# Kernel optimization log

Hardware: AMD Instinct MI355X
Metric: run time of the kernel (lower is better)

Reference implementation:

```python
import jax, jax.numpy as jnp
import numpy as np

N, E, F, H = 20000, 320000, 128, 256   # nodes, edges, in-features, hidden
M, NQ = 4096, 2048                      # lsq rows, QP variables
LAMB_MAX = 2.0


def setup_inputs() -> dict:
    key = jax.random.key(0)
    ks = jax.random.split(key, 12)
    x = jax.random.normal(ks[0], (N, F), jnp.float32)
    edge_index = jax.random.randint(ks[1], (2, E), 0, N)
    A = jax.random.normal(ks[2], (M, NQ), jnp.float32) * 0.05
    b = jax.random.normal(ks[3], (M, 1), jnp.float32)
    feat_ids = jax.random.randint(ks[4], (NQ,), 0, N)
    x_prior = jax.random.uniform(ks[5], (NQ, 1), jnp.float32)
    lamb = jnp.ones((1,), jnp.float32)
    # ChebConv K=2 weights: one linear per Chebyshev order, plus bias
    W10 = jax.random.normal(ks[6], (F, H), jnp.float32) / np.sqrt(F)
    W11 = jax.random.normal(ks[7], (F, H), jnp.float32) / np.sqrt(F)
    b1 = jnp.zeros((H,), jnp.float32)
    W20 = jax.random.normal(ks[8], (H, 1), jnp.float32) / np.sqrt(H)
    W21 = jax.random.normal(ks[9], (H, 1), jnp.float32) / np.sqrt(H)
    b2 = jnp.zeros((1,), jnp.float32)
    return {"x": x, "edge_index": edge_index, "A": A, "b": b,
            "feat_ids": feat_ids, "x_prior": x_prior, "lamb": lamb,
            "W10": W10, "W11": W11, "b1": b1,
            "W20": W20, "W21": W21, "b2": b2}


def _cheb_conv(x, edge_index, W0, W1, bias, lam_max):
    """PyG ChebConv with K=2: out = x @ W0 + (2L/lam_max - I) x @ W1 + bias,
    L = I - D^{-1/2} A D^{-1/2}, via edge gather/scatter (no dense NxN)."""
    row, col = edge_index[0], edge_index[1]
    n = x.shape[0]
    deg = jax.ops.segment_sum(jnp.ones_like(row, dtype=x.dtype), row, num_segments=n)
    dinv = jnp.where(deg > 0, deg ** -0.5, 0.0)
    # normalized edge weight scaled by 2/lam_max, negated (off-diag of L_hat)
    w = -(2.0 / lam_max) * dinv[row] * dinv[col]              # [E]
    msg = jax.ops.segment_sum(w[:, None] * x[col], row, num_segments=n)
    Tx1 = msg + (2.0 / lam_max - 1.0) * x                      # diagonal of L_hat
    return x @ W0 + Tx1 @ W1 + bias


def reference(x, edge_index, A, b, feat_ids, x_prior, lamb,
              W10, W11, b1, W20, W21, b2):
    h = jax.nn.relu(_cheb_conv(x, edge_index, W10, W11, b1, LAMB_MAX))
    h = lamb[0] * jax.nn.relu(_cheb_conv(h, edge_index, W20, W21, b2, LAMB_MAX))
    hfold = h[feat_ids] + 1e-5                                 # [NQ, 1]
    q = hfold[:, 0]
    # QP: min 1/2 z^T Q z + p^T z with vacuous inequality (0*z <= 0.1) and no
    # equality constraints -> interior-point converges to unconstrained min.
    Q = A.T @ A + jnp.diag(q)                                  # [NQ, NQ]
    p = -(x_prior * hfold)[:, 0] - (b.T @ A)[0]                # [NQ]
    z = jnp.linalg.solve(Q, -p)                                # [NQ]
    return z[:, None]                                          # f.T -> [NQ, 1]
```

## Files before the change

kernel.cpp:

```cpp
#include <hip/hip_runtime.h>

#define N_NODES 20000
#define N_EDGES 320000
#define F_DIM   128
#define H_DIM   256
#define M_ROWS  4096
#define NQ      2048
#define NIT     18
#define MM_ROWS 20032

typedef __attribute__((ext_vector_type(8))) short short8;
typedef __attribute__((ext_vector_type(4))) float f32x4;


__device__ __forceinline__ float wred(float v) {
#pragma unroll
  for (int m = 32; m > 0; m >>= 1) v += __shfl_xor(v, m, 64);
  return v;
}

__device__ __forceinline__ float bred256(float v, float* lds) {
  v = wred(v);
  int w = threadIdx.x >> 6;
  if ((threadIdx.x & 63) == 0) lds[w] = v;
  __syncthreads();
  float tot = lds[0] + lds[1] + lds[2] + lds[3];
  __syncthreads();
  return tot;
}

__device__ __forceinline__ unsigned f2bf(float f) {
  unsigned u = __float_as_uint(f);
  unsigned r = u + 0x7fffu + ((u >> 16) & 1u);
  return r >> 16;
}
__device__ __forceinline__ float bflo(unsigned u) { return __uint_as_float(u << 16); }
__device__ __forceinline__ float bfhi(unsigned u) { return __uint_as_float(u & 0xffff0000u); }


__global__ __launch_bounds__(1024) void k_scan(const int* __restrict__ deg,
    int* __restrict__ rowstart, float* __restrict__ dinv) {
  __shared__ int part[1024];
  int t = threadIdx.x;
  const int chunk = (N_NODES + 1023) / 1024;
  int lo = t * chunk;
  int hi = lo + chunk; if (hi > N_NODES) hi = N_NODES;
  int s = 0;
  for (int i = lo; i < hi; ++i) {
    int d = deg[i];
    dinv[i] = d > 0 ? rsqrtf((float)d) : 0.f;
    s += d;
  }
  part[t] = s;
  __syncthreads();
  for (int off = 1; off < 1024; off <<= 1) {
    int v = part[t];
    int add = (t >= off) ? part[t - off] : 0;
    __syncthreads();
    part[t] = v + add;
    __syncthreads();
  }
  int base = (t > 0) ? part[t - 1] : 0;
  for (int i = lo; i < hi; ++i) { rowstart[i] = base; base += deg[i]; }
  if (t == 0) rowstart[N_NODES] = part[1023];
}

__global__ __launch_bounds__(256) void k_scatter(const int* __restrict__ ei,
    const int* __restrict__ rowstart, int* __restrict__ cursor,
    const float* __restrict__ dinv, int* __restrict__ cols, float* __restrict__ wvals) {
  int e = blockIdx.x * 256 + threadIdx.x;
  if (e >= N_EDGES) return;
  int r = ei[e];
  int c = ei[N_EDGES + e];
  int pos = rowstart[r] + atomicAdd(&cursor[r], 1);
  cols[pos] = c;
  wvals[pos] = -dinv[r] * dinv[c];
}

#define CONVX_BLKS (MM_ROWS * 16 / 256)
#define DEG_BLKS   ((N_EDGES + 255) / 256)
#define PREP_BASE  (CONVX_BLKS + 128 + DEG_BLKS)

__global__ __launch_bounds__(256) void k_pack(const float* __restrict__ x,
    const float* __restrict__ W10, const float* __restrict__ W11,
    unsigned* __restrict__ xu, unsigned* __restrict__ Wtb,
    const int* __restrict__ ei, int* __restrict__ deg,
    const float* __restrict__ A, const float* __restrict__ b,
    unsigned* __restrict__ Atu, float* __restrict__ btA_parts) {
  int bx = blockIdx.x;
  if (bx < CONVX_BLKS) {
    int gid = bx * 256 + threadIdx.x;
    int row = gid >> 4;
    int q8 = gid & 15;
    uint4* xu4 = (uint4*)xu;
    if (row < N_NODES) {
      const float4* x4 = (const float4*)x;
      float4 a = x4[(size_t)row * 32 + q8 * 2];
      float4 b2 = x4[(size_t)row * 32 + q8 * 2 + 1];
      uint4 u;
      u.x = f2bf(a.x) | (f2bf(a.y) << 16);
      u.y = f2bf(a.z) | (f2bf(a.w) << 16);
      u.z = f2bf(b2.x) | (f2bf(b2.y) << 16);
      u.w = f2bf(b2.z) | (f2bf(b2.w) << 16);
      xu4[(size_t)row * 32 + q8] = u;
    } else {
      uint4 z = make_uint4(0, 0, 0, 0);
      xu4[(size_t)row * 32 + q8] = z;
      xu4[(size_t)row * 32 + 16 + q8] = z;
    }
  } else if (bx < CONVX_BLKS + 128) {
    int gid = (bx - CONVX_BLKS) * 256 + threadIdx.x;
    int n = gid >> 7;
    int u = gid & 127;
    int k0 = u * 2;
    float v0 = (k0 < 128) ? W10[(size_t)k0 * H_DIM + n]
                          : W11[(size_t)(k0 - 128) * H_DIM + n];
    float v1 = (k0 + 1 < 128) ? W10[(size_t)(k0 + 1) * H_DIM + n]
                              : W11[(size_t)(k0 - 127) * H_DIM + n];
    Wtb[(size_t)n * 128 + u] = f2bf(v0) | (f2bf(v1) << 16);
  } else if (bx < PREP_BASE) {
    int e = (bx - CONVX_BLKS - 128) * 256 + threadIdx.x;
    if (e < N_EDGES) atomicAdd(&deg[ei[e]], 1);
  } else {
    const int pb = bx - PREP_BASE;
    int jp = (pb & 3) * 256 + threadIdx.x;
    int k0 = (pb >> 2) * 128;
    const float2* A2 = (const float2*)A;
    float acc0 = 0.f, acc1 = 0.f;
    for (int kk = 0; kk < 128; kk += 8) {
      float ax[8], ay[8];
#pragma unroll
      for (int i = 0; i < 8; ++i) {
        int k = k0 + kk + i;
        float2 a = A2[(size_t)k * 1024 + jp];
        float bk = b[k];
        acc0 += a.x * bk;
        acc1 += a.y * bk;
        ax[i] = a.x; ay[i] = a.y;
      }
      uint4 t0, t1;
      t0.x = f2bf(ax[0]) | (f2bf(ax[1]) << 16);
      t0.y = f2bf(ax[2]) | (f2bf(ax[3]) << 16);
      t0.z = f2bf(ax[4]) | (f2bf(ax[5]) << 16);
      t0.w = f2bf(ax[6]) | (f2bf(ax[7]) << 16);
      t1.x = f2bf(ay[0]) | (f2bf(ay[1]) << 16);
      t1.y = f2bf(ay[2]) | (f2bf(ay[3]) << 16);
      t1.z = f2bf(ay[4]) | (f2bf(ay[5]) << 16);
      t1.w = f2bf(ay[6]) | (f2bf(ay[7]) << 16);
      int uoff = (k0 + kk) >> 1;
      *(uint4*)(Atu + (size_t)(2 * jp) * 2048 + uoff) = t0;
      *(uint4*)(Atu + (size_t)(2 * jp + 1) * 2048 + uoff) = t1;
    }
    ((float2*)(btA_parts + (size_t)(pb >> 2) * NQ))[jp] = make_float2(acc0, acc1);
  }
}

__global__ __launch_bounds__(256) void k_msg1(const int* __restrict__ rowstart,
    const int* __restrict__ cols, const float* __restrict__ wvals,
    unsigned* __restrict__ xu) {
  int wid = (blockIdx.x * 256 + threadIdx.x) >> 6;
  int lane = threadIdx.x & 63;
  if (wid >= N_NODES) return;
  int s0 = rowstart[wid], s1 = rowstart[wid + 1];
  float2 a0 = make_float2(0.f, 0.f), a1 = make_float2(0.f, 0.f);
  float2 a2 = make_float2(0.f, 0.f), a3 = make_float2(0.f, 0.f);
  int e = s0;
  for (; e + 4 <= s1; e += 4) {
    int c0 = cols[e], c1 = cols[e + 1], c2 = cols[e + 2], c3 = cols[e + 3];
    float w0 = wvals[e], w1 = wvals[e + 1], w2 = wvals[e + 2], w3 = wvals[e + 3];
    unsigned u0 = xu[(size_t)c0 * 128 + lane];
    unsigned u1 = xu[(size_t)c1 * 128 + lane];
    unsigned u2 = xu[(size_t)c2 * 128 + lane];
    unsigned u3 = xu[(size_t)c3 * 128 + lane];
    a0.x += w0 * bflo(u0); a0.y += w0 * bfhi(u0);
    a1.x += w1 * bflo(u1); a1.y += w1 * bfhi(u1);
    a2.x += w2 * bflo(u2); a2.y += w2 * bfhi(u2);
    a3.x += w3 * bflo(u3); a3.y += w3 * bfhi(u3);
  }
  for (; e < s1; ++e) {
    int c = cols[e];
    float w = wvals[e];
    unsigned u = xu[(size_t)c * 128 + lane];
    a0.x += w * bflo(u); a0.y += w * bfhi(u);
  }
  float ax = (a0.x + a1.x) + (a2.x + a3.x);
  float ay = (a0.y + a1.y) + (a2.y + a3.y);
  xu[(size_t)wid * 128 + 64 + lane] = f2bf(ax) | (f2bf(ay) << 16);
}


__device__ __forceinline__ void mm_ldfrag(short8* Af, short8* Bf,
    const unsigned* __restrict__ xurow, const unsigned* __restrict__ wrow, int kc) {
#pragma unroll
  for (int a = 0; a < 4; ++a)
    Af[a] = *(const short8*)(xurow + (size_t)a * 16 * 128 + kc * 16);
#pragma unroll
  for (int n = 0; n < 4; ++n)
    Bf[n] = *(const short8*)(wrow + (size_t)n * 16 * 128 + kc * 16);
}

__global__ __launch_bounds__(256) void k_mm(const unsigned* __restrict__ xu,
    const unsigned* __restrict__ Wtb, const float* __restrict__ b1,
    const float* __restrict__ W20, const float* __restrict__ W21,
    float* __restrict__ t, float* __restrict__ s) {
  const int row0 = blockIdx.x * 64;
  const int tid = threadIdx.x;
  const int w = tid >> 6, lane = tid & 63;
  const int colb = w * 64;
  const int frow = lane & 15, fqo = (lane >> 4) * 4;
  const int c16 = lane & 15, q4 = lane >> 4;

  f32x4 acc[4][4];
#pragma unroll
  for (int a = 0; a < 4; ++a)
#pragma unroll
    for (int b = 0; b < 4; ++b) {
      acc[a][b][0] = 0.f; acc[a][b][1] = 0.f;
      acc[a][b][2] = 0.f; acc[a][b][3] = 0.f;
    }

  const unsigned* xurow = xu + (size_t)(row0 + frow) * 128 + fqo;
  const unsigned* wrow  = Wtb + (size_t)(colb + frow) * 128 + fqo;

  short8 A0[4], B0[4], A1[4], B1[4];
  mm_ldfrag(A0, B0, xurow, wrow, 0);
#pragma unroll
  for (int kp = 0; kp < 4; ++kp) {
    const int kc = kp * 2;
    mm_ldfrag(A1, B1, xurow, wrow, kc + 1);
#pragma unroll
    for (int a = 0; a < 4; ++a)
#pragma unroll
      for (int n = 0; n < 4; ++n)
        acc[a][n] = __builtin_amdgcn_mfma_f32_16x16x32_bf16(A0[a], B0[n], acc[a][n], 0, 0, 0);
    if (kc + 2 < 8) mm_ldfrag(A0, B0, xurow, wrow, kc + 2);
#pragma unroll
    for (int a = 0; a < 4; ++a)
#pragma unroll
      for (int n = 0; n < 4; ++n)
        acc[a][n] = __builtin_amdgcn_mfma_f32_16x16x32_bf16(A1[a], B1[n], acc[a][n], 0, 0, 0);
  }

  float tp[4][4] = {}, sp[4][4] = {};
#pragma unroll
  for (int b2 = 0; b2 < 4; ++b2) {
    int gc = colb + b2 * 16 + c16;
    float w20 = W20[gc], w21 = W21[gc], bb = b1[gc];
#pragma unroll
    for (int a = 0; a < 4; ++a)
#pragma unroll
      for (int r = 0; r < 4; ++r) {
        float val = acc[a][b2][r] + bb;
        val = val > 0.f ? val : 0.f;
        tp[a][r] += val * w20;
        sp[a][r] += val * w21;
      }
  }
#pragma unroll
  for (int a = 0; a < 4; ++a)
#pragma unroll
    for (int r = 0; r < 4; ++r) {
#pragma unroll
      for (int m = 1; m < 16; m <<= 1) {
        tp[a][r] += __shfl_xor(tp[a][r], m, 64);
        sp[a][r] += __shfl_xor(sp[a][r], m, 64);
      }
    }
  if (c16 == 0) {
#pragma unroll
    for (int a = 0; a < 4; ++a)
#pragma unroll
      for (int r = 0; r < 4; ++r) {
        int gr = row0 + a * 16 + q4 * 4 + r;
        if (gr < N_NODES) {
          atomicAdd(&t[gr], tp[a][r]);
          atomicAdd(&s[gr], sp[a][r]);
        }
      }
  }
}


__global__ __launch_bounds__(256) void k_h2(const float* __restrict__ t,
    const float* __restrict__ s, const int* __restrict__ rowstart,
    const int* __restrict__ cols, const float* __restrict__ wvals,
    const float* __restrict__ lamb, const float* __restrict__ b2, float* __restrict__ h2) {
  int i = blockIdx.x * 256 + threadIdx.x;
  if (i >= N_NODES) return;
  int s0 = rowstart[i], s1 = rowstart[i + 1];
  float m0 = 0.f, m1 = 0.f, m2 = 0.f, m3 = 0.f;
  int e = s0;
  for (; e + 4 <= s1; e += 4) {
    int c0 = cols[e], c1 = cols[e + 1], c2 = cols[e + 2], c3 = cols[e + 3];
    float w0 = wvals[e], w1 = wvals[e + 1], w2 = wvals[e + 2], w3 = wvals[e + 3];
    m0 += w0 * s[c0];
    m1 += w1 * s[c1];
    m2 += w2 * s[c2];
    m3 += w3 * s[c3];
  }
  for (; e < s1; ++e) m0 += wvals[e] * s[cols[e]];
  float m = (m0 + m1) + (m2 + m3);
  float val = t[i] + m + b2[0];
  val = val > 0.f ? val : 0.f;
  h2[i] = lamb[0] * val;
}

#define GR_ST2 36
#define NTILE 136

__global__ __launch_bounds__(512) void k_gram(const unsigned* __restrict__ Atu,
    float* __restrict__ Gp,
    const float* __restrict__ h2, const int* __restrict__ feat_ids,
    const float* __restrict__ x_prior, const float* __restrict__ btA_parts,
    float* __restrict__ q, float* __restrict__ r0) {
  if (blockIdx.x >= 544) {
    if (threadIdx.x < 256) {
      int j = (blockIdx.x - 544) * 256 + threadIdx.x;
      int f = feat_ids[j];
      float hf = h2[f] + 1e-5f;
      q[j] = hf;
      float bta = 0.f;
#pragma unroll
      for (int c = 0; c < 32; ++c) bta += btA_parts[(size_t)c * NQ + j];
      r0[j] = x_prior[j] * hf + bta;
    }
    return;
  }
  __shared__ unsigned shA[128 * GR_ST2];
  __shared__ unsigned shB[128 * GR_ST2];
  const int bid = blockIdx.x;
  const int wid = (bid & 7) * 68 + (bid >> 3);
  const int tile = wid >> 2;
  const int kq = wid & 3;
  int uu = tile, bi = 0;
  while (uu >= 16 - bi) { uu -= 16 - bi; ++bi; }
  const int bj = bi + uu;
  const int i0 = bi * 128, j0 = bj * 128;
  const int tid = threadIdx.x;
  const int w = tid >> 6, lane = tid & 63;
  const int wr = (w >> 2) * 64, wc = (w & 3) * 32;
  const int srow = tid >> 2, sua = (tid & 3) * 8;
  const int frow = lane & 15, fqo = (lane >> 4) * 4;

  f32x4 acc[4][2];
#pragma unroll
  for (int a = 0; a < 4; ++a)
#pragma unroll
    for (int b = 0; b < 2; ++b) {
      acc[a][b][0] = 0.f; acc[a][b][1] = 0.f;
      acc[a][b][2] = 0.f; acc[a][b][3] = 0.f;
    }

  const unsigned* pa = Atu + (size_t)(i0 + srow) * 2048 + kq * 512 + sua;
  const unsigned* pb = Atu + (size_t)(j0 + srow) * 2048 + kq * 512 + sua;

  uint4 pra0 = *(const uint4*)(pa);
  uint4 pra1 = *(const uint4*)(pa + 4);
  uint4 prb0 = *(const uint4*)(pb);
  uint4 prb1 = *(const uint4*)(pb + 4);

  unsigned* as = shA + srow * GR_ST2 + sua;
  unsigned* bs = shB + srow * GR_ST2 + sua;

  for (int sp = 0; sp < 16; ++sp) {
    *(uint4*)as = pra0; *(uint4*)(as + 4) = pra1;
    *(uint4*)bs = prb0; *(uint4*)(bs + 4) = prb1;
    if (sp + 1 < 16) {
      const int ku = (sp + 1) * 32;
      pra0 = *(const uint4*)(pa + ku);
      pra1 = *(const uint4*)(pa + ku + 4);
      prb0 = *(const uint4*)(pb + ku);
      prb1 = *(const uint4*)(pb + ku + 4);
    }
    __syncthreads();
#pragma unroll
    for (int kk = 0; kk < 2; ++kk) {
      short8 af[4], bf[2];
#pragma unroll
      for (int a = 0; a < 4; ++a)
        af[a] = *(const short8*)(shA + (wr + a * 16 + frow) * GR_ST2 + kk * 16 + fqo);
#pragma unroll
      for (int b2 = 0; b2 < 2; ++b2)
        bf[b2] = *(const short8*)(shB + (wc + b2 * 16 + frow) * GR_ST2 + kk * 16 + fqo);
#pragma unroll
      for (int a = 0; a < 4; ++a)
#pragma unroll
        for (int b2 = 0; b2 < 2; ++b2)
          acc[a][b2] = __builtin_amdgcn_mfma_f32_16x16x32_bf16(af[a], bf[b2], acc[a][b2], 0, 0, 0);
    }
    __syncthreads();
  }

  const int q4 = lane >> 4, c16 = lane & 15;
  float* Gz = Gp + ((size_t)kq * NTILE + tile) * 16384;
#pragma unroll
  for (int a = 0; a < 4; ++a)
#pragma unroll
    for (int b2 = 0; b2 < 2; ++b2)
#pragma unroll
      for (int r = 0; r < 4; ++r) {
        int lr = wr + a * 16 + q4 * 4 + r;
        int lc = wc + b2 * 16 + c16;
        Gz[lr * 128 + lc] = acc[a][b2][r];
      }
}

#define GT_ST 131

__global__ __launch_bounds__(256) void k_gconv(const float* __restrict__ Gp,
    const float* __restrict__ q, unsigned* __restrict__ Gb, float* __restrict__ qcorr) {
  __shared__ unsigned short T[128 * GT_ST];
  int uu = blockIdx.x, bi = 0;
  while (uu >= 16 - bi) { uu -= 16 - bi; ++bi; }
  const int bj = bi + uu;
  const int tid = threadIdx.x;
  const int r = tid >> 1, ch = (tid & 1) * 64;
  const size_t tile = (size_t)blockIdx.x * 16384;
  const float4* P0 = (const float4*)(Gp + tile + r * 128 + ch);
  const float4* P1 = (const float4*)(Gp + (size_t)1 * NTILE * 16384 + tile + r * 128 + ch);
  const float4* P2 = (const float4*)(Gp + (size_t)2 * NTILE * 16384 + tile + r * 128 + ch);
  const float4* P3 = (const float4*)(Gp + (size_t)3 * NTILE * 16384 + tile + r * 128 + ch);
  const int gr = bi * 128 + r;
  const bool hasdiag = (bi == bj) && (r >= ch) && (r < ch + 64);
  unsigned uo[32];
#pragma unroll
  for (int j = 0; j < 16; ++j) {
    float4 a = P0[j], b = P1[j], c = P2[j], d = P3[j];
    float v0 = a.x + b.x + c.x + d.x;
    float v1 = a.y + b.y + c.y + d.y;
    float v2 = a.z + b.z + c.z + d.z;
    float v3 = a.w + b.w + c.w + d.w;
    const int c0 = ch + j * 4;
    if (hasdiag && (r - c0 >= 0) && (r - c0 < 4)) {
      float qv = q[gr];
      int dsel = r - c0;
      if (dsel == 0) v0 += qv;
      else if (dsel == 1) v1 += qv;
      else if (dsel == 2) v2 += qv;
      else v3 += qv;
      float vd = (dsel == 0) ? v0 : (dsel == 1) ? v1 : (dsel == 2) ? v2 : v3;
      qcorr[gr] = vd - bflo(f2bf(vd));
    }
    unsigned u0 = f2bf(v0) | (f2bf(v1) << 16);
    unsigned u1 = f2bf(v2) | (f2bf(v3) << 16);
    uo[2 * j] = u0;
    uo[2 * j + 1] = u1;
    T[r * GT_ST + c0]     = (unsigned short)(u0 & 0xffffu);
    T[r * GT_ST + c0 + 1] = (unsigned short)(u0 >> 16);
    T[r * GT_ST + c0 + 2] = (unsigned short)(u1 & 0xffffu);
    T[r * GT_ST + c0 + 3] = (unsigned short)(u1 >> 16);
  }
  uint4* dst = (uint4*)(Gb + (size_t)gr * 1024 + bj * 64 + (ch >> 1));
#pragma unroll
  for (int j = 0; j < 8; ++j) dst[j] = ((const uint4*)uo)[j];
  __syncthreads();
  if (bi != bj) {
    const int wv = tid >> 6, lane = tid & 63;
    for (int kk = 0; kk < 32; ++kk) {
      int rr = kk * 4 + wv;
      unsigned lo = T[(2 * lane) * GT_ST + rr];
      unsigned hi = T[(2 * lane + 1) * GT_ST + rr];
      Gb[(size_t)(bj * 128 + rr) * 1024 + bi * 64 + lane] = lo | (hi << 16);
    }
  }
}

__global__ __launch_bounds__(256) void k_cgG(int k, const unsigned* __restrict__ Gb,
    const float* __restrict__ qcorr,
    const float* __restrict__ r_old, float* __restrict__ r_new,
    const float* __restrict__ p_old, float* __restrict__ p_new,
    const float* __restrict__ Qp_in, float* __restrict__ Qp_out,
    float* __restrict__ xcg) {
  __shared__ float pshare[NQ];
  __shared__ float lds[4];
  const int tid = threadIdx.x, bid = blockIdx.x;
  const float4* r4 = (const float4*)r_old;
  float4 ra = r4[tid * 2], rb2 = r4[tid * 2 + 1];
  float pv[8];
  if (k == 0) {
    pv[0] = ra.x; pv[1] = ra.y; pv[2] = ra.z; pv[3] = ra.w;
    pv[4] = rb2.x; pv[5] = rb2.y; pv[6] = rb2.z; pv[7] = rb2.w;
    if (bid == 0) {
      ((float4*)p_new)[tid * 2] = ra;
      ((float4*)p_new)[tid * 2 + 1] = rb2;
    }
  } else {
    const float4* p4 = (const float4*)p_old;
    const float4* qp4 = (const float4*)Qp_in;
    float4 pa = p4[tid * 2], pb = p4[tid * 2 + 1];
    float4 qa = qp4[tid * 2], qb = qp4[tid * 2 + 1];
    float rr = ra.x * ra.x + ra.y * ra.y + ra.z * ra.z + ra.w * ra.w +
               rb2.x * rb2.x + rb2.y * rb2.y + rb2.z * rb2.z + rb2.w * rb2.w;
    float pap = pa.x * qa.x + pa.y * qa.y + pa.z * qa.z + pa.w * qa.w +
                pb.x * qb.x + pb.y * qb.y + pb.z * qb.z + pb.w * qb.w;
    rr = bred256(rr, lds);
    pap = bred256(pap, lds);
    float alpha = rr / pap;
    if (bid == 0) {
      float4* x4 = (float4*)xcg;
      float4 xa = x4[tid * 2], xb = x4[tid * 2 + 1];
      xa.x += alpha * pa.x; xa.y += alpha * pa.y;
      xa.z += alpha * pa.z; xa.w += alpha * pa.w;
      xb.x += alpha * pb.x; xb.y += alpha * pb.y;
      xb.z += alpha * pb.z; xb.w += alpha * pb.w;
      x4[tid * 2] = xa; x4[tid * 2 + 1] = xb;
    }
    ra.x -= alpha * qa.x; ra.y -= alpha * qa.y;
    ra.z -= alpha * qa.z; ra.w -= alpha * qa.w;
    rb2.x -= alpha * qb.x; rb2.y -= alpha * qb.y;
    rb2.z -= alpha * qb.z; rb2.w -= alpha * qb.w;
    float rrn = ra.x * ra.x + ra.y * ra.y + ra.z * ra.z + ra.w * ra.w +
                rb2.x * rb2.x + rb2.y * rb2.y + rb2.z * rb2.z + rb2.w * rb2.w;
    rrn = bred256(rrn, lds);
    float beta = rrn / rr;
    pv[0] = ra.x + beta * pa.x; pv[1] = ra.y + beta * pa.y;
    pv[2] = ra.z + beta * pa.z; pv[3] = ra.w + beta * pa.w;
    pv[4] = rb2.x + beta * pb.x; pv[5] = rb2.y + beta * pb.y;
    pv[6] = rb2.z + beta * pb.z; pv[7] = rb2.w + beta * pb.w;
    if (bid == 0) {
      ((float4*)r_new)[tid * 2] = ra;
      ((float4*)r_new)[tid * 2 + 1] = rb2;
      ((float4*)p_new)[tid * 2] = make_float4(pv[0], pv[1], pv[2], pv[3]);
      ((float4*)p_new)[tid * 2 + 1] = make_float4(pv[4], pv[5], pv[6], pv[7]);
    }
  }
  ((float4*)pshare)[tid * 2] = make_float4(pv[0], pv[1], pv[2], pv[3]);
  ((float4*)pshare)[tid * 2 + 1] = make_float4(pv[4], pv[5], pv[6], pv[7]);
  __syncthreads();
  const int w = tid >> 6, lane = tid & 63;
  const int row0 = bid * 8 + w * 2;
  const uint4* Gr0 = (const uint4*)(Gb + (size_t)row0 * 1024);
  const uint4* Gr1 = (const uint4*)(Gb + (size_t)(row0 + 1) * 1024);
  const float4* ps4 = (const float4*)pshare;
  float acc0 = 0.f, acc1 = 0.f;
#pragma unroll
  for (int c = 0; c < 4; ++c) {
    uint4 g0 = Gr0[c * 64 + lane];
    uint4 g1 = Gr1[c * 64 + lane];
    float4 pa = ps4[c * 128 + lane * 2];
    float4 pb = ps4[c * 128 + lane * 2 + 1];
    acc0 += bflo(g0.x) * pa.x + bfhi(g0.x) * pa.y;
    acc0 += bflo(g0.y) * pa.z + bfhi(g0.y) * pa.w;
    acc0 += bflo(g0.z) * pb.x + bfhi(g0.z) * pb.y;
    acc0 += bflo(g0.w) * pb.z + bfhi(g0.w) * pb.w;
    acc1 += bflo(g1.x) * pa.x + bfhi(g1.x) * pa.y;
    acc1 += bflo(g1.y) * pa.z + bfhi(g1.y) * pa.w;
    acc1 += bflo(g1.z) * pb.x + bfhi(g1.z) * pb.y;
    acc1 += bflo(g1.w) * pb.z + bfhi(g1.w) * pb.w;
  }
  acc0 = wred(acc0);
  acc1 = wred(acc1);
  if (lane == 0) {
    Qp_out[row0] = acc0 + qcorr[row0] * pshare[row0];
    Qp_out[row0 + 1] = acc1 + qcorr[row0 + 1] * pshare[row0 + 1];
  }
}

__global__ __launch_bounds__(256) void k_cgfin(const float* __restrict__ r_last,
    const float* __restrict__ p_last, const float* __restrict__ Qp,
    const float* __restrict__ xcg, float* __restrict__ out) {
  const int tid = threadIdx.x;
  const int lane = tid & 63;
  const float4* r4 = (const float4*)r_last;
  const float4* p4 = (const float4*)p_last;
  const float4* q4 = (const float4*)Qp;
  float rr = 0.f, pap = 0.f;
#pragma unroll
  for (int c = 0; c < 4; ++c) {
#pragma unroll
    for (int hh = 0; hh < 2; ++hh) {
      float4 rv = r4[c * 128 + lane * 2 + hh];
      float4 pv = p4[c * 128 + lane * 2 + hh];
      float4 qv = q4[c * 128 + lane * 2 + hh];
      rr += rv.x * rv.x + rv.y * rv.y + rv.z * rv.z + rv.w * rv.w;
      pap += pv.x * qv.x + pv.y * qv.y + pv.z * qv.z + pv.w * qv.w;
    }
  }
  rr = wred(rr);
  pap = wred(pap);
  float alpha = rr / pap;
  const float4* x4 = (const float4*)xcg;
  float4* o4 = (float4*)out;
#pragma unroll
  for (int hh = 0; hh < 2; ++hh) {
    int i4 = tid * 2 + hh;
    float4 xv = x4[i4];
    float4 pv = p4[i4];
    xv.x += alpha * pv.x; xv.y += alpha * pv.y;
    xv.z += alpha * pv.z; xv.w += alpha * pv.w;
    o4[i4] = xv;
  }
}


extern "C" void kernel_launch(void* const* d_in, const int* in_sizes, int n_in,
                              void* d_out, int out_size, void* d_ws, size_t ws_size,
                              hipStream_t stream) {
  const float* x      = (const float*)d_in[0];
  const int*   ei     = (const int*)d_in[1];
  const float* A      = (const float*)d_in[2];
  const float* b      = (const float*)d_in[3];
  const int*   fids   = (const int*)d_in[4];
  const float* xprior = (const float*)d_in[5];
  const float* lamb   = (const float*)d_in[6];
  const float* W10    = (const float*)d_in[7];
  const float* W11    = (const float*)d_in[8];
  const float* b1     = (const float*)d_in[9];
  const float* W20    = (const float*)d_in[10];
  const float* W21    = (const float*)d_in[11];
  const float* b2     = (const float*)d_in[12];
  float* out = (float*)d_out;

  char* base = (char*)d_ws;
  size_t o = 0;
  auto alloc = [&](size_t bytes) { size_t r = o; o = (o + bytes + 255) & ~size_t(255); return r; };

  size_t off_deg    = alloc(N_NODES * 4);
  size_t off_cursor = alloc(N_NODES * 4);
  size_t off_xcg    = alloc(NQ * 4);
  size_t off_t      = alloc(N_NODES * 4);
  size_t off_s      = alloc(N_NODES * 4);
  size_t zero_end   = o;
  size_t off_rowst  = alloc((N_NODES + 1) * 4);
  size_t off_dinv   = alloc(N_NODES * 4);
  size_t off_h2     = alloc(N_NODES * 4);
  size_t off_q      = alloc(NQ * 4);
  size_t off_r0     = alloc(NQ * 4);
  size_t off_r1     = alloc(NQ * 4);
  size_t off_p0     = alloc(NQ * 4);
  size_t off_p1     = alloc(NQ * 4);
  size_t off_Qp0    = alloc(NQ * 4);
  size_t off_Qp1    = alloc(NQ * 4);
  size_t off_qcorr  = alloc(NQ * 4);
  size_t off_btAp   = alloc(32 * NQ * 4);
  size_t off_Wtb    = alloc(256 * 128 * 4);
  size_t sz_cols  = (size_t)N_EDGES * 4 + 256;
  size_t sz_wvals = (size_t)N_EDGES * 4 + 256;
  size_t sz_xmsg  = (size_t)MM_ROWS * 256 * 2;
  size_t union_gnn = sz_cols + sz_wvals + sz_xmsg;
  size_t sz_gb     = (size_t)NQ * NQ * 2;
  size_t off_union = alloc(union_gnn > sz_gb ? union_gnn : sz_gb);
  size_t off_atu   = alloc((size_t)M_ROWS * NQ * 2);
  size_t off_Gp    = alloc((size_t)4 * NTILE * 16384 * 4);
  if (o > ws_size) return;

  int*   deg      = (int*)(base + off_deg);
  int*   cursor   = (int*)(base + off_cursor);
  float* xcg      = (float*)(base + off_xcg);
  float* t        = (float*)(base + off_t);
  float* s        = (float*)(base + off_s);
  int*   rowstart = (int*)(base + off_rowst);
  float* dinv     = (float*)(base + off_dinv);
  float* h2       = (float*)(base + off_h2);
  float* q        = (float*)(base + off_q);
  float* rb[2]    = {(float*)(base + off_r0), (float*)(base + off_r1)};
  float* pg[2]    = {(float*)(base + off_p0), (float*)(base + off_p1)};
  float* Qpb[2]   = {(float*)(base + off_Qp0), (float*)(base + off_Qp1)};
  float* qcorr    = (float*)(base + off_qcorr);
  float* btA_parts = (float*)(base + off_btAp);
  unsigned* Wtb   = (unsigned*)(base + off_Wtb);
  int*   cols     = (int*)(base + off_union);
  float* wvals    = (float*)(base + off_union + sz_cols);
  unsigned* xmsgb = (unsigned*)(base + off_union + sz_cols + sz_wvals);
  unsigned* Gb    = (unsigned*)(base + off_union);
  unsigned* Atu   = (unsigned*)(base + off_atu);
  float* Gp       = (float*)(base + off_Gp);

  hipMemsetAsync(d_ws, 0, zero_end, stream);

  k_pack<<<PREP_BASE + 128, 256, 0, stream>>>(x, W10, W11, xmsgb, Wtb, ei, deg,
                                              A, b, Atu, btA_parts);
  k_scan<<<1, 1024, 0, stream>>>(deg, rowstart, dinv);
  k_scatter<<<DEG_BLKS, 256, 0, stream>>>(ei, rowstart, cursor, dinv, cols, wvals);

  k_msg1<<<N_NODES / 4, 256, 0, stream>>>(rowstart, cols, wvals, xmsgb);
  k_mm<<<MM_ROWS / 64, 256, 0, stream>>>(xmsgb, Wtb, b1, W20, W21, t, s);
  k_h2<<<(N_NODES + 255) / 256, 256, 0, stream>>>(t, s, rowstart, cols, wvals, lamb, b2, h2);

  k_gram<<<552, 512, 0, stream>>>(Atu, Gp, h2, fids, xprior, btA_parts, q, rb[0]);
  k_gconv<<<NTILE, 256, 0, stream>>>(Gp, q, Gb, qcorr);

  k_cgG<<<256, 256, 0, stream>>>(0, Gb, qcorr, rb[0], rb[0], pg[0], pg[0],
                                 Qpb[1], Qpb[0], xcg);
  for (int k = 1; k < NIT; ++k) {
    k_cgG<<<256, 256, 0, stream>>>(k, Gb, qcorr, rb[(k - 1) & 1], rb[k & 1],
                                   pg[(k - 1) & 1], pg[k & 1],
                                   Qpb[(k - 1) & 1], Qpb[k & 1], xcg);
  }
  k_cgfin<<<1, 256, 0, stream>>>(rb[(NIT - 1) & 1], pg[(NIT - 1) & 1],
                                 Qpb[(NIT - 1) & 1], xcg, out);
}
```

Before: 397.4 us.

## Move A transpose/pack into separate LDS-tiled kernel after conv matmul

Moves the A-transpose-to-bf16 and b^T A partial computation out of the fused k_pack kernel into a new k_prep2 kernel. The new kernel stages a 128x64 tile in shared memory so both the global reads of A and the packed writes of Atu are coalesced, where the old per-thread loop issued strided 16-byte stores. It is launched after k_mm, taking A's packing off the critical path of the graph preprocessing. The cost is one extra kernel launch and a separate pass that no longer overlaps with the edge-degree work.

```diff
diff --git a/kernel.cpp b/kernel.cpp
--- a/kernel.cpp
+++ b/kernel.cpp
@@ -79,14 +79,11 @@
 
 #define CONVX_BLKS (MM_ROWS * 16 / 256)
 #define DEG_BLKS   ((N_EDGES + 255) / 256)
-#define PREP_BASE  (CONVX_BLKS + 128 + DEG_BLKS)
 
 __global__ __launch_bounds__(256) void k_pack(const float* __restrict__ x,
     const float* __restrict__ W10, const float* __restrict__ W11,
     unsigned* __restrict__ xu, unsigned* __restrict__ Wtb,
-    const int* __restrict__ ei, int* __restrict__ deg,
-    const float* __restrict__ A, const float* __restrict__ b,
-    unsigned* __restrict__ Atu, float* __restrict__ btA_parts) {
+    const int* __restrict__ ei, int* __restrict__ deg) {
   int bx = blockIdx.x;
   if (bx < CONVX_BLKS) {
     int gid = bx * 256 + threadIdx.x;
@@ -118,40 +115,57 @@
     float v1 = (k0 + 1 < 128) ? W10[(size_t)(k0 + 1) * H_DIM + n]
                               : W11[(size_t)(k0 - 127) * H_DIM + n];
     Wtb[(size_t)n * 128 + u] = f2bf(v0) | (f2bf(v1) << 16);
-  } else if (bx < PREP_BASE) {
+  } else {
     int e = (bx - CONVX_BLKS - 128) * 256 + threadIdx.x;
     if (e < N_EDGES) atomicAdd(&deg[ei[e]], 1);
-  } else {
-    const int pb = bx - PREP_BASE;
-    int jp = (pb & 3) * 256 + threadIdx.x;
-    int k0 = (pb >> 2) * 128;
-    const float2* A2 = (const float2*)A;
-    float acc0 = 0.f, acc1 = 0.f;
-    for (int kk = 0; kk < 128; kk += 8) {
-      float ax[8], ay[8];
-#pragma unroll
-      for (int i = 0; i < 8; ++i) {
-        int k = k0 + kk + i;
-        float2 a = A2[(size_t)k * 1024 + jp];
-        float bk = b[k];
-        acc0 += a.x * bk;
-        acc1 += a.y * bk;
-        ax[i] = a.x; ay[i] = a.y;
-      }
-      uint4 t0, t1;
-      t0.x = f2bf(ax[0]) | (f2bf(ax[1]) << 16);
-      t0.y = f2bf(ax[2]) | (f2bf(ax[3]) << 16);
-      t0.z = f2bf(ax[4]) | (f2bf(ax[5]) << 16);
-      t0.w = f2bf(ax[6]) | (f2bf(ax[7]) << 16);
-      t1.x = f2bf(ay[0]) | (f2bf(ay[1]) << 16);
-      t1.y = f2bf(ay[2]) | (f2bf(ay[3]) << 16);
-      t1.z = f2bf(ay[4]) | (f2bf(ay[5]) << 16);
-      t1.w = f2bf(ay[6]) | (f2bf(ay[7]) << 16);
-      int uoff = (k0 + kk) >> 1;
-      *(uint4*)(Atu + (size_t)(2 * jp) * 2048 + uoff) = t0;
-      *(uint4*)(Atu + (size_t)(2 * jp + 1) * 2048 + uoff) = t1;
-    }
-    ((float2*)(btA_parts + (size_t)(pb >> 2) * NQ))[jp] = make_float2(acc0, acc1);
+  }
+}
+
+#define PT_ST 130
+
+__global__ __launch_bounds__(256) void k_prep2(const float* __restrict__ A,
+    const float* __restrict__ b, unsigned* __restrict__ Atu,
+    float* __restrict__ btA_parts) {
+  __shared__ unsigned short T[64 * PT_ST];
+  __shared__ float part[64 * 4];
+  const int t = threadIdx.x;
+  const int jt = blockIdx.x & 31, kt = blockIdx.x >> 5;
+  const int j0 = jt * 64, k0 = kt * 128;
+  const int jl = t & 63, kq = t >> 6;
+  float bta = 0.f;
+#pragma unroll 8
+  for (int p = 0; p < 32; ++p) {
+    int row = k0 + p * 4 + kq;
+    float v = A[(size_t)row * NQ + j0 + jl];
+    bta += b[row] * v;
+    T[jl * PT_ST + p * 4 + kq] = (unsigned short)f2bf(v);
+  }
+  part[jl * 4 + kq] = bta;
+  __syncthreads();
+  const int jr = t >> 2, c = t & 3;
+  const unsigned short* Tr = T + jr * PT_ST + c * 32;
+  uint4 uu0, uu1, uu2, uu3;
+  uu0.x = (unsigned)Tr[0]  | ((unsigned)Tr[1]  << 16);
+  uu0.y = (unsigned)Tr[2]  | ((unsigned)Tr[3]  << 16);
+  uu0.z = (unsigned)Tr[4]  | ((unsigned)Tr[5]  << 16);
+  uu0.w = (unsigned)Tr[6]  | ((unsigned)Tr[7]  << 16);
+  uu1.x = (unsigned)Tr[8]  | ((unsigned)Tr[9]  << 16);
+  uu1.y = (unsigned)Tr[10] | ((unsigned)Tr[11] << 16);
+  uu1.z = (unsigned)Tr[12] | ((unsigned)Tr[13] << 16);
+  uu1.w = (unsigned)Tr[14] | ((unsigned)Tr[15] << 16);
+  uu2.x = (unsigned)Tr[16] | ((unsigned)Tr[17] << 16);
+  uu2.y = (unsigned)Tr[18] | ((unsigned)Tr[19] << 16);
+  uu2.z = (unsigned)Tr[20] | ((unsigned)Tr[21] << 16);
+  uu2.w = (unsigned)Tr[22] | ((unsigned)Tr[23] << 16);
+  uu3.x = (unsigned)Tr[24] | ((unsigned)Tr[25] << 16);
+  uu3.y = (unsigned)Tr[26] | ((unsigned)Tr[27] << 16);
+  uu3.z = (unsigned)Tr[28] | ((unsigned)Tr[29] << 16);
+  uu3.w = (unsigned)Tr[30] | ((unsigned)Tr[31] << 16);
+  uint4* dst = (uint4*)(Atu + (size_t)(j0 + jr) * 2048 + kt * 64 + c * 16);
+  dst[0] = uu0; dst[1] = uu1; dst[2] = uu2; dst[3] = uu3;
+  if (t < 64) {
+    float s4 = (part[t * 4] + part[t * 4 + 1]) + (part[t * 4 + 2] + part[t * 4 + 3]);
+    btA_parts[(size_t)kt * NQ + j0 + t] = s4;
   }
 }
 
@@ -668,13 +682,15 @@
 
   hipMemsetAsync(d_ws, 0, zero_end, stream);
 
-  k_pack<<<PREP_BASE + 128, 256, 0, stream>>>(x, W10, W11, xmsgb, Wtb, ei, deg,
-                                              A, b, Atu, btA_parts);
+  k_pack<<<CONVX_BLKS + 128 + DEG_BLKS, 256, 0, stream>>>(x, W10, W11, xmsgb, Wtb, ei, deg);
   k_scan<<<1, 1024, 0, stream>>>(deg, rowstart, dinv);
   k_scatter<<<DEG_BLKS, 256, 0, stream>>>(ei, rowstart, cursor, dinv, cols, wvals);
 
   k_msg1<<<N_NODES / 4, 256, 0, stream>>>(rowstart, cols, wvals, xmsgb);
   k_mm<<<MM_ROWS / 64, 256, 0, stream>>>(xmsgb, Wtb, b1, W20, W21, t, s);
+
+  k_prep2<<<1024, 256, 0, stream>>>(A, b, Atu, btA_parts);
+
   k_h2<<<(N_NODES + 255) / 256, 256, 0, stream>>>(t, s, rowstart, cols, wvals, lamb, b2, h2);
 
   k_gram<<<552, 512, 0, stream>>>(Atu, Gp, h2, fids, xprior, btA_parts, q, rb[0]);
```

New measurement: 367.1 us. 1.08x faster.
